# Kernel tuning notes

Hardware: AMD Instinct MI355X
Metric: run time of the kernel (lower is better)

## Reference

```python
import jax, jax.numpy as jnp
import numpy as np

EPS = 1e-6
CHUNK = 128  # chunk size for the causal linear-attention scan


def elu_plus_one(x):
    return jax.nn.elu(x) + 1.0


def causal_linear_attention(q, k, v):
    # out_t = (sq_t @ cumsum_{j<=t} sk_j v_j^T) / (sq_t . cumsum_{j<=t} sk_j), clamped
    B, S, D = q.shape
    sq = elu_plus_one(q)
    sk = elu_plus_one(k)
    N = S // CHUNK
    # [N, B, C, D] chunked layout for scan over chunks
    sq_c = sq.reshape(B, N, CHUNK, D).transpose(1, 0, 2, 3)
    sk_c = sk.reshape(B, N, CHUNK, D).transpose(1, 0, 2, 3)
    v_c = v.reshape(B, N, CHUNK, D).transpose(1, 0, 2, 3)
    mask = jnp.tril(jnp.ones((CHUNK, CHUNK), dtype=q.dtype))  # inclusive causal

    def step(carry, inp):
        S_kv, z = carry  # [B,D,D], [B,D] running sums from previous chunks
        sqi, ski, vi = inp
        A = jnp.einsum('bid,bjd->bij', sqi, ski) * mask  # intra-chunk causal scores
        num = jnp.einsum('bij,bje->bie', A, vi) + jnp.einsum('bid,bde->bie', sqi, S_kv)
        den = A.sum(-1) + jnp.einsum('bid,bd->bi', sqi, z)
        out = num / jnp.clip(den, EPS, None)[..., None]
        S_kv = S_kv + jnp.einsum('bcd,bce->bde', ski, vi)
        z = z + ski.sum(axis=1)
        return (S_kv, z), out

    init = (jnp.zeros((B, D, D), q.dtype), jnp.zeros((B, D), q.dtype))
    _, outs = jax.lax.scan(step, init, (sq_c, sk_c, v_c))
    return outs.transpose(1, 0, 2, 3).reshape(B, S, D)


def setup_inputs() -> dict:
    key = jax.random.key(0)
    ks = jax.random.split(key, 8)
    B, S, D = 2, 2048, 1024
    scale = 1.0 / np.sqrt(D)  # realistic init scale for the D x D projections
    return {
        'hidden_states': jax.random.normal(ks[0], (B, S, D), jnp.float32),
        'w_q': jax.random.normal(ks[1], (D, D), jnp.float32) * scale,
        'w_k': jax.random.normal(ks[2], (D, D), jnp.float32) * scale,
        'w_v': jax.random.normal(ks[3], (D, D), jnp.float32) * scale,
        'w_o': jax.random.normal(ks[4], (D, D), jnp.float32) * scale,
        'gate': jnp.zeros((1,), jnp.float32),
        'memory': jax.random.uniform(ks[5], (D, D), jnp.float32) * 0.01,
        'memory_norm': jax.random.uniform(ks[6], (D,), jnp.float32),
    }


def reference(hidden_states, w_q, w_k, w_v, w_o, gate, memory, memory_norm):
    # Projections (torch Linear: x @ W^T)
    q = hidden_states @ w_q.T
    k = hidden_states @ w_k.T
    v = hidden_states @ w_v.T

    # Retrieve from compressive memory (single bank)
    sigma_q = elu_plus_one(q)
    a_mem = sigma_q @ memory
    norm = jnp.clip(sigma_q @ memory_norm, EPS, None)[..., None]
    active = (memory_norm.sum() >= EPS).astype(q.dtype)
    memory_output = active * (a_mem / norm)

    local_output = causal_linear_attention(q, k, v)

    g = jax.nn.sigmoid(gate)  # [1], broadcasts
    output = g * memory_output + (1.0 - g) * local_output
    return output @ w_o.T
```

## Files before the change

### kernel.cpp

```cpp
#include <hip/hip_runtime.h>
#include <cstddef>

#define EPSF 1e-6f

constexpr int D   = 1024;
constexpr int Bv  = 2;
constexpr int S   = 2048;
constexpr int M   = Bv * S;
constexpr int CH  = 256;
constexpr int NCH = S / CH;

constexpr int TSZ  = 128 * 32;
constexpr int TA64 = 64 * 32;

typedef __attribute__((ext_vector_type(8))) short short8;
typedef __attribute__((ext_vector_type(4))) float floatx4;

__device__ __forceinline__ float elu1(float x) { return x > 0.f ? x + 1.f : __expf(x); }
__device__ __forceinline__ float sigmoidf_(float x) { return 1.f / (1.f + __expf(-x)); }
__device__ __forceinline__ unsigned short f2bf(float x) {
    unsigned u = __float_as_uint(x);
    return (unsigned short)((u + 0x7fffu + ((u >> 16) & 1u)) >> 16);
}
__device__ __forceinline__ float bf2f(unsigned short h) {
    return __uint_as_float(((unsigned)h) << 16);
}
__device__ __forceinline__ float wave_reduce(float x) {
#pragma unroll
    for (int off = 32; off > 0; off >>= 1) x += __shfl_down(x, off);
    return x;
}

__device__ __forceinline__ void gl_lds16(const unsigned short* g, unsigned short* l) {
    __builtin_amdgcn_global_load_lds(
        (const __attribute__((address_space(1))) void*)g,
        (__attribute__((address_space(3))) void*)l, 16, 0, 0);
}


__device__ __forceinline__ void stage128x32(const unsigned short* g, int stride,
                                            unsigned short* lds, int wave, int lane) {
    const int t   = (wave << 6) + lane;
    const int row = t >> 2;
    const int cb  = (((t & 3) ^ ((row >> 1) & 3)) << 3);
    unsigned short* l0 = lds + (wave << 9);
    gl_lds16(g + (size_t)row * stride + cb, l0);
    gl_lds16(g + (size_t)(row + 64) * stride + cb, l0 + 2048);
}

__device__ __forceinline__ void stage64x32(const unsigned short* g, int stride,
                                           unsigned short* lds, int wave, int lane) {
    const int t   = (wave << 6) + lane;
    const int row = t >> 2;
    const int cb  = (((t & 3) ^ ((row >> 1) & 3)) << 3);
    gl_lds16(g + (size_t)row * stride + cb, lds + (wave << 9));
}

__device__ __forceinline__ void mfma_step(const unsigned short* As, const unsigned short* Bs,
                                          int wm, int wn, int fr, int g, floatx4 acc[4][4]) {
    const int off = ((g ^ ((fr >> 1) & 3)) << 3);
    short8 af[4], bf[4];
#pragma unroll
    for (int i = 0; i < 4; ++i) af[i] = *(const short8*)&As[(wm + i * 16 + fr) * 32 + off];
#pragma unroll
    for (int j = 0; j < 4; ++j) bf[j] = *(const short8*)&Bs[(wn + j * 16 + fr) * 32 + off];
#pragma unroll
    for (int i = 0; i < 4; ++i)
#pragma unroll
        for (int j = 0; j < 4; ++j)
            acc[i][j] = __builtin_amdgcn_mfma_f32_16x16x32_bf16(af[i], bf[j], acc[i][j], 0, 0, 0);
}

__device__ __forceinline__ void mfma_step64d(const unsigned short* As, const unsigned short* Bs,
                                             int wm, int wn, int fr, int g,
                                             floatx4 acc[2][4], floatx4 accd[2], short8 bones) {
    const int off = ((g ^ ((fr >> 1) & 3)) << 3);
    short8 af[2], bf[4];
#pragma unroll
    for (int i = 0; i < 2; ++i) af[i] = *(const short8*)&As[(wm + i * 16 + fr) * 32 + off];
#pragma unroll
    for (int j = 0; j < 4; ++j) bf[j] = *(const short8*)&Bs[(wn + j * 16 + fr) * 32 + off];
#pragma unroll
    for (int i = 0; i < 2; ++i) {
#pragma unroll
        for (int j = 0; j < 4; ++j)
            acc[i][j] = __builtin_amdgcn_mfma_f32_16x16x32_bf16(af[i], bf[j], acc[i][j], 0, 0, 0);
        accd[i] = __builtin_amdgcn_mfma_f32_16x16x32_bf16(af[i], bones, accd[i], 0, 0, 0);
    }
}

__device__ __forceinline__ void mfma_step64(const unsigned short* As, const unsigned short* Bs,
                                            int wm, int wn, int fr, int g, floatx4 acc[2][4]) {
    const int off = ((g ^ ((fr >> 1) & 3)) << 3);
    short8 af[2], bf[4];
#pragma unroll
    for (int i = 0; i < 2; ++i) af[i] = *(const short8*)&As[(wm + i * 16 + fr) * 32 + off];
#pragma unroll
    for (int j = 0; j < 4; ++j) bf[j] = *(const short8*)&Bs[(wn + j * 16 + fr) * 32 + off];
#pragma unroll
    for (int i = 0; i < 2; ++i)
#pragma unroll
        for (int j = 0; j < 4; ++j)
            acc[i][j] = __builtin_amdgcn_mfma_f32_16x16x32_bf16(af[i], bf[j], acc[i][j], 0, 0, 0);
}

__device__ __forceinline__ void gemm_loop_db(const unsigned short* Ag, int strideA,
                                             const unsigned short* Bg, int strideB, int Kk,
                                             unsigned short* As, unsigned short* Bs,
                                             int wave, int lane, int wm, int wn, int fr, int g,
                                             floatx4 acc[4][4]) {
    __syncthreads();
    stage128x32(Ag, strideA, As, wave, lane);
    stage128x32(Bg, strideB, Bs, wave, lane);
    int buf = 0;
    for (int k0 = 32; k0 < Kk; k0 += 32) {
        __syncthreads();
        const int nb = buf ^ 1;
        stage128x32(Ag + k0, strideA, As + nb * TSZ, wave, lane);
        stage128x32(Bg + k0, strideB, Bs + nb * TSZ, wave, lane);
        mfma_step(As + buf * TSZ, Bs + buf * TSZ, wm, wn, fr, g, acc);
        buf = nb;
    }
    __syncthreads();
    mfma_step(As + buf * TSZ, Bs + buf * TSZ, wm, wn, fr, g, acc);
}

__device__ __forceinline__ void gemm_loop_db64d(const unsigned short* Ag, int strideA,
                                                const unsigned short* Bg, int strideB, int Kk,
                                                unsigned short* As, unsigned short* Bs,
                                                int wave, int lane, int wm, int wn, int fr, int g,
                                                floatx4 acc[2][4], floatx4 accd[2], short8 bones) {
    __syncthreads();
    stage64x32(Ag, strideA, As, wave, lane);
    stage128x32(Bg, strideB, Bs, wave, lane);
    int buf = 0;
    for (int k0 = 32; k0 < Kk; k0 += 32) {
        __syncthreads();
        const int nb = buf ^ 1;
        stage64x32(Ag + k0, strideA, As + nb * TA64, wave, lane);
        stage128x32(Bg + k0, strideB, Bs + nb * TSZ, wave, lane);
        mfma_step64d(As + buf * TA64, Bs + buf * TSZ, wm, wn, fr, g, acc, accd, bones);
        buf = nb;
    }
    __syncthreads();
    mfma_step64d(As + buf * TA64, Bs + buf * TSZ, wm, wn, fr, g, acc, accd, bones);
}

__device__ __forceinline__ void gemm_loop_db64(const unsigned short* Ag, int strideA,
                                               const unsigned short* Bg, int strideB, int Kk,
                                               unsigned short* As, unsigned short* Bs,
                                               int wave, int lane, int wm, int wn, int fr, int g,
                                               floatx4 acc[2][4]) {
    __syncthreads();
    stage64x32(Ag, strideA, As, wave, lane);
    stage128x32(Bg, strideB, Bs, wave, lane);
    int buf = 0;
    for (int k0 = 32; k0 < Kk; k0 += 32) {
        __syncthreads();
        const int nb = buf ^ 1;
        stage64x32(Ag + k0, strideA, As + nb * TA64, wave, lane);
        stage128x32(Bg + k0, strideB, Bs + nb * TSZ, wave, lane);
        mfma_step64(As + buf * TA64, Bs + buf * TSZ, wm, wn, fr, g, acc);
        buf = nb;
    }
    __syncthreads();
    mfma_step64(As + buf * TA64, Bs + buf * TSZ, wm, wn, fr, g, acc);
}

__global__ __launch_bounds__(256) void prep(const float* __restrict__ h,
                                            const float* __restrict__ w_q, const float* __restrict__ w_k,
                                            const float* __restrict__ w_v, const float* __restrict__ w_o,
                                            const float* __restrict__ memory,
                                            unsigned short* __restrict__ h_b,
                                            unsigned short* __restrict__ wq_b, unsigned short* __restrict__ wk_b,
                                            unsigned short* __restrict__ wv_b, unsigned short* __restrict__ wo_b,
                                            unsigned short* __restrict__ memT)
{
    __shared__ unsigned short T[64][72];
    const int id = blockIdx.x, tid = threadIdx.x;
    if (id < 4096) {
        const size_t i = ((size_t)id * 256 + tid) * 4;
        float4 v = *(const float4*)(h + i);
        ushort4 o; o.x = f2bf(v.x); o.y = f2bf(v.y); o.z = f2bf(v.z); o.w = f2bf(v.w);
        *(ushort4*)(h_b + i) = o;
    } else if (id < 8192) {
        const int t = id - 4096, which = t >> 10;
        const float* in = (which == 0) ? w_q : (which == 1) ? w_k : (which == 2) ? w_v : w_o;
        unsigned short* out = (which == 0) ? wq_b : (which == 1) ? wk_b : (which == 2) ? wv_b : wo_b;
        const size_t i = ((size_t)(t & 1023) * 256 + tid) * 4;
        float4 v = *(const float4*)(in + i);
        ushort4 o; o.x = f2bf(v.x); o.y = f2bf(v.y); o.z = f2bf(v.z); o.w = f2bf(v.w);
        *(ushort4*)(out + i) = o;
    } else {
        const int t = id - 8192;
        const int d0 = (t >> 4) * 64, e0 = (t & 15) * 64;
        const int r = tid >> 4, c4 = (tid & 15) * 4;
        for (int rr = r; rr < 64; rr += 16) {
            float4 v = *(const float4*)(memory + (size_t)(d0 + rr) * D + e0 + c4);
            T[rr][c4 + 0] = f2bf(v.x); T[rr][c4 + 1] = f2bf(v.y);
            T[rr][c4 + 2] = f2bf(v.z); T[rr][c4 + 3] = f2bf(v.w);
        }
        __syncthreads();
        for (int rr = r; rr < 64; rr += 16) {
            ushort4 o;
            o.x = T[c4 + 0][rr]; o.y = T[c4 + 1][rr];
            o.z = T[c4 + 2][rr]; o.w = T[c4 + 3][rr];
            *(ushort4*)(memT + (size_t)(e0 + rr) * D + d0 + c4) = o;
        }
    }
}

__global__ __launch_bounds__(256) void proj_fused(const unsigned short* __restrict__ h_b,
                                                  const unsigned short* __restrict__ wq,
                                                  const unsigned short* __restrict__ wk,
                                                  const unsigned short* __restrict__ wv,
                                                  unsigned short* __restrict__ sq,
                                                  unsigned short* __restrict__ sk,
                                                  unsigned short* __restrict__ v)
{
    __shared__ unsigned short As[2 * TSZ], Bs[2 * TSZ];
    const int id = blockIdx.x;
    const int x = id & 7, y = id >> 3;
    const int strip = x + 8 * (y % 12);
    const int n     = y / 12;
    const int sub = strip >> 5, m = strip & 31;
    const int m0 = m * 128, n0 = n * 128;
    const unsigned short* B = (sub == 0) ? wq : (sub == 1) ? wk : wv;
    unsigned short* C = (sub == 0) ? sq : (sub == 1) ? sk : v;

    const int tid = threadIdx.x, wave = tid >> 6, lane = tid & 63;
    const int wm = (wave >> 1) * 64, wn = (wave & 1) * 64;
    const int fr = lane & 15, g = lane >> 4;
    const int q4 = g * 4;

    floatx4 acc[4][4] = {};
    gemm_loop_db(h_b + (size_t)m0 * D, D, B + (size_t)n0 * D, D, D,
                 As, Bs, wave, lane, wm, wn, fr, g, acc);

#pragma unroll
    for (int i = 0; i < 4; ++i)
#pragma unroll
        for (int j = 0; j < 4; ++j) {
            const int col = n0 + wn + j * 16 + fr;
#pragma unroll
            for (int r = 0; r < 4; ++r) {
                const int row = m0 + wm + i * 16 + q4 + r;
                float val = acc[i][j][r];
                if (sub < 2) val = elu1(val);
                C[(size_t)row * D + col] = f2bf(val);
            }
        }
}

__global__ __launch_bounds__(256) void stage2(const unsigned short* __restrict__ sq,
                                              const unsigned short* __restrict__ sk,
                                              const unsigned short* __restrict__ memT,
                                              const unsigned short* __restrict__ v_b,
                                              const float* __restrict__ mnorm,
                                              const float* __restrict__ gate,
                                              unsigned short* __restrict__ combm,
                                              unsigned short* __restrict__ Sbuf2,
                                              unsigned short* __restrict__ vT,
                                              float* __restrict__ rowscale)
{
    __shared__ unsigned short As[2 * TSZ], Bs[2 * TSZ];
    const int id = blockIdx.x, tid = threadIdx.x;
    const int wave = tid >> 6, lane = tid & 63;
    const int wm = (wave >> 1) * 64, wn = (wave & 1) * 64;
    const int fr = lane & 15, g = lane >> 4;
    const int q4 = g * 4;

    if (id < 256) {
        const int x = id & 7, y = id >> 3;
        const int m0 = (x + 8 * (y & 3)) * 128;
        const int n0 = (y >> 2) * 128;
        floatx4 acc[4][4] = {};
        gemm_loop_db(sq + (size_t)m0 * D, D, memT + (size_t)n0 * D, D, D,
                     As, Bs, wave, lane, wm, wn, fr, g, acc);
#pragma unroll
        for (int i = 0; i < 4; ++i)
#pragma unroll
            for (int j = 0; j < 4; ++j) {
                const int col = n0 + wn + j * 16 + fr;
#pragma unroll
                for (int r = 0; r < 4; ++r)
                    combm[(size_t)(m0 + wm + i * 16 + q4 + r) * D + col] = f2bf(acc[i][j][r]);
            }
    } else if (id < 544) {
        const int t = id - 256;
        const int b = t / 144, rem = t % 144;
        const int p = rem >> 2, tt = rem & 3;
        const int it = tt >> 1, jt = tt & 1;
        int c = 0;
        while ((c + 1) * (c + 2) / 2 <= p) ++c;
        const int j = p - c * (c + 1) / 2;
        unsigned short* Srow0 = Sbuf2 + (size_t)(b * NCH + c) * CH * S;

        if (j == c && jt > it) {
            const int row = it * 128 + (tid >> 1);
            unsigned short* zp = Srow0 + (size_t)row * S + j * CH + jt * 128 + (tid & 1) * 64;
            uint4 z4 = make_uint4(0, 0, 0, 0);
#pragma unroll
            for (int i = 0; i < 8; ++i) *(uint4*)(zp + i * 8) = z4;
            return;
        }
        floatx4 acc[4][4] = {};
        gemm_loop_db(sq + ((size_t)b * S + (size_t)c * CH + it * 128) * D, D,
                     sk + ((size_t)b * S + (size_t)j * CH + jt * 128) * D, D, D,
                     As, Bs, wave, lane, wm, wn, fr, g, acc);
        const bool diag = (j == c && it == jt);
#pragma unroll
        for (int i = 0; i < 4; ++i)
#pragma unroll
            for (int jj = 0; jj < 4; ++jj) {
                const int col = jt * 128 + wn + jj * 16 + fr;
#pragma unroll
                for (int r = 0; r < 4; ++r) {
                    const int row = it * 128 + wm + i * 16 + q4 + r;
                    float val = acc[i][jj][r];
                    if (diag && col > row) val = 0.f;
                    Srow0[(size_t)row * S + j * CH + col] = f2bf(val);
                }
            }
    } else if (id < 1568) {
        unsigned short (*T)[72] = (unsigned short(*)[72])As;
        const int t = id - 544;
        const int b = t >> 9, rem = t & 511;
        const int s0 = (rem >> 4) * 64, d0 = (rem & 15) * 64;
        const int r = tid >> 4, c4 = (tid & 15) * 4;
        const unsigned short* ip = v_b + (size_t)b * S * D;
        for (int rr = r; rr < 64; rr += 16) {
            ushort4 vv = *(const ushort4*)(ip + (size_t)(s0 + rr) * D + d0 + c4);
            T[rr][c4 + 0] = vv.x; T[rr][c4 + 1] = vv.y; T[rr][c4 + 2] = vv.z; T[rr][c4 + 3] = vv.w;
        }
        __syncthreads();
        unsigned short* op = vT + (size_t)b * D * S;
        for (int rr = r; rr < 64; rr += 16) {
            ushort4 o;
            o.x = T[c4 + 0][rr]; o.y = T[c4 + 1][rr];
            o.z = T[c4 + 2][rr]; o.w = T[c4 + 3][rr];
            *(ushort4*)(op + (size_t)(d0 + rr) * S + s0 + c4) = o;
        }
    } else {
        const int row = (id - 1568) * 4 + wave;
        const unsigned short* sr = sq + (size_t)row * D;
        float dot = 0.f, msum = 0.f;
        for (int d = lane; d < D; d += 64) {
            float mn = mnorm[d];
            dot += bf2f(sr[d]) * mn;
            msum += mn;
        }
        dot = wave_reduce(dot);
        msum = wave_reduce(msum);
        if (lane == 0) {
            const float gg = sigmoidf_(gate[0]);
            const float active = (msum >= EPSF) ? 1.f : 0.f;
            rowscale[row] = gg * active / fmaxf(dot, EPSF);
        }
    }
}

__global__ __launch_bounds__(256) void pv64(const unsigned short* __restrict__ Sbuf2,
                                            const unsigned short* __restrict__ vT,
                                            const float* __restrict__ rowscale,
                                            const float* __restrict__ gate,
                                            unsigned short* __restrict__ combm)
{
    __shared__ unsigned short As2[2 * TA64], Bs2[2 * TSZ];
    const int id = blockIdx.x, tid = threadIdx.x;
    const int wave = tid >> 6, lane = tid & 63;
    const int wm = (wave >> 1) * 32, wn = (wave & 1) * 64;
    const int fr = lane & 15, g = lane >> 4;
    const int q4 = g * 4;

    const int x = id & 7, y = id >> 3;
    const int g_ = x + 8 * (y & 7);
    const int e  = y >> 3;
    const int b = g_ >> 5;
    const int rem = g_ & 31;
    const int c = (NCH - 1) - (rem >> 2);
    const int i0 = (rem & 3) * 64, e0 = e * 128;

    const short one_bf = (short)0x3F80;
    short8 bones = {one_bf, one_bf, one_bf, one_bf, one_bf, one_bf, one_bf, one_bf};

    floatx4 acc[2][4] = {};
    floatx4 accd[2] = {};
    gemm_loop_db64d(Sbuf2 + ((size_t)(b * NCH + c) * CH + i0) * S, S,
                    vT + (size_t)b * D * S + (size_t)e0 * S, S, (c + 1) * CH,
                    As2, Bs2, wave, lane, wm, wn, fr, g, acc, accd, bones);

    const float gg = sigmoidf_(gate[0]);
    const float wloc = 1.f - gg;
#pragma unroll
    for (int i = 0; i < 2; ++i)
#pragma unroll
        for (int j = 0; j < 4; ++j) {
            const int col = e0 + wn + j * 16 + fr;
#pragma unroll
            for (int r = 0; r < 4; ++r) {
                const int li = i0 + wm + i * 16 + q4 + r;
                const int rg = b * S + c * CH + li;
                const float inv = wloc / fmaxf(accd[i][r], EPSF);
                const size_t idx = (size_t)rg * D + col;
                combm[idx] = f2bf(bf2f(combm[idx]) * rowscale[rg] + acc[i][j][r] * inv);
            }
        }
}

__global__ __launch_bounds__(256) void outproj64(const unsigned short* __restrict__ A,
                                                 const unsigned short* __restrict__ wo,
                                                 float* __restrict__ out)
{
    __shared__ unsigned short As2[2 * TA64], Bs2[2 * TSZ];
    const int id = blockIdx.x, tid = threadIdx.x;
    const int wave = tid >> 6, lane = tid & 63;
    const int wm = (wave >> 1) * 32, wn = (wave & 1) * 64;
    const int fr = lane & 15, g = lane >> 4;
    const int q4 = g * 4;

    const int x = id & 7, y = id >> 3;
    const int m0 = (x + 8 * (y & 7)) * 64;
    const int n0 = (y >> 3) * 128;

    floatx4 acc[2][4] = {};
    gemm_loop_db64(A + (size_t)m0 * D, D, wo + (size_t)n0 * D, D, D,
                   As2, Bs2, wave, lane, wm, wn, fr, g, acc);

#pragma unroll
    for (int i = 0; i < 2; ++i)
#pragma unroll
        for (int j = 0; j < 4; ++j) {
            const int col = n0 + wn + j * 16 + fr;
#pragma unroll
            for (int r = 0; r < 4; ++r)
                out[(size_t)(m0 + wm + i * 16 + q4 + r) * D + col] = acc[i][j][r];
        }
}

extern "C" void kernel_launch(void* const* d_in, const int* in_sizes, int n_in,
                              void* d_out, int out_size, void* d_ws, size_t ws_size,
                              hipStream_t stream)
{
    const float* h      = (const float*)d_in[0];
    const float* w_q    = (const float*)d_in[1];
    const float* w_k    = (const float*)d_in[2];
    const float* w_v    = (const float*)d_in[3];
    const float* w_o    = (const float*)d_in[4];
    const float* gate   = (const float*)d_in[5];
    const float* memory = (const float*)d_in[6];
    const float* mnorm  = (const float*)d_in[7];
    float* out = (float*)d_out;

    unsigned short* h_b   = (unsigned short*)d_ws;
    unsigned short* wq_b  = h_b + (size_t)M * D;
    unsigned short* wk_b  = wq_b + (size_t)D * D;
    unsigned short* wv_b  = wk_b + (size_t)D * D;
    unsigned short* wo_b  = wv_b + (size_t)D * D;
    unsigned short* memT  = wo_b + (size_t)D * D;
    unsigned short* sq_b  = memT + (size_t)D * D;
    unsigned short* sk_b  = sq_b + (size_t)M * D;
    unsigned short* v_b   = sk_b + (size_t)M * D;
    unsigned short* vT    = v_b + (size_t)M * D;
    unsigned short* Sbuf2 = vT + (size_t)M * D;
    unsigned short* combm = Sbuf2 + (size_t)Bv * NCH * CH * S;
    float* rowscale = (float*)(combm + (size_t)M * D);

    dim3 blk(256);

    prep<<<8448, blk, 0, stream>>>(h, w_q, w_k, w_v, w_o, memory,
                                   h_b, wq_b, wk_b, wv_b, wo_b, memT);
    proj_fused<<<768, blk, 0, stream>>>(h_b, wq_b, wk_b, wv_b, sq_b, sk_b, v_b);
    stage2<<<2592, blk, 0, stream>>>(sq_b, sk_b, memT, v_b, mnorm, gate,
                                     combm, Sbuf2, vT, rowscale);
    pv64<<<512, blk, 0, stream>>>(Sbuf2, vT, rowscale, gate, combm);
    outproj64<<<512, blk, 0, stream>>>(combm, wo_b, out);
}
```

Measured before the change: 230.3 us.

## Replace QKV projection with 256x256-tile 8-wave GEMM using 128KB dynamic LDS

Adds a new projection kernel that computes 256x256 output tiles with 512 threads (8 waves, each 128x64). It uses 64-wide K steps, a double-buffered 128KB LDS pipeline staged via global_load_lds with XOR swizzle, interleaved prefetch, and setprio around the MFMA bursts. The larger tiles are meant to raise arithmetic intensity and cut global/LDS traffic compared with the 128x128 proj_fused, which is kept as a fallback if the large dynamic LDS request fails. Separately, the rowscale dot product is vectorized into 16-byte loads. Risks include low occupancy and only 192 blocks, which may underfill the CUs.

Result: no change. 227.2 us (-1.4%).

```diff
diff --git a/kernel.cpp b/kernel.cpp
--- a/kernel.cpp
+++ b/kernel.cpp
@@ -36,7 +36,6 @@
         (const __attribute__((address_space(1))) void*)g,
         (__attribute__((address_space(3))) void*)l, 16, 0, 0);
 }
-
 
 __device__ __forceinline__ void stage128x32(const unsigned short* g, int stride,
                                             unsigned short* lds, int wave, int lane) {
@@ -210,6 +209,122 @@
     }
 }
 
+__global__ __launch_bounds__(512, 2) void proj8(const unsigned short* __restrict__ h_b,
+                                                const unsigned short* __restrict__ wq,
+                                                const unsigned short* __restrict__ wk,
+                                                const unsigned short* __restrict__ wv,
+                                                unsigned short* __restrict__ sq,
+                                                unsigned short* __restrict__ sk,
+                                                unsigned short* __restrict__ v)
+{
+    extern __shared__ unsigned short sm[];
+    const int id = blockIdx.x;
+    const int x = id & 7, y = id >> 3;
+    const int strip = x + 8 * (y % 6);
+    const int nn = y / 6;
+    const int sub = strip >> 4, m = strip & 15;
+    const int m0 = m * 256, n0 = nn * 256;
+    const unsigned short* Ag = h_b + (size_t)m0 * D;
+    const unsigned short* Bg = ((sub == 0) ? wq : (sub == 1) ? wk : wv) + (size_t)n0 * D;
+    unsigned short* C = (sub == 0) ? sq : (sub == 1) ? sk : v;
+
+    const int tid = threadIdx.x;
+    const int w = tid >> 6, lane = tid & 63;
+    const int wr = w >> 2, wc = w & 3;
+    const int fr = lane & 15, gq = lane >> 4;
+    const int swz = fr & 7;
+
+    const int r0 = tid >> 3;
+    const int c0 = (tid & 7) ^ (r0 & 7);
+    const int r1 = (tid + 512) >> 3;
+    const int c1 = ((tid + 512) & 7) ^ (r1 & 7);
+    const size_t so0 = (size_t)r0 * D + (size_t)c0 * 8;
+    const size_t so1 = (size_t)r1 * D + (size_t)c1 * 8;
+    unsigned short* const dst0 = sm + tid * 8;
+    unsigned short* const dst1 = sm + (tid + 512) * 8;
+
+    floatx4 acc[8][4] = {};
+
+#define STG(kt, b, which) do {                                                      \
+        const unsigned short* Gs = ((which) < 2 ? Ag : Bg)                          \
+            + (size_t)(((which) & 1) * 128) * D + (size_t)(kt) * 64;                \
+        const int slot = (((b) << 2) + (which)) << 13;                              \
+        gl_lds16(Gs + so0, dst0 + slot);                                            \
+        gl_lds16(Gs + so1, dst1 + slot);                                            \
+    } while (0)
+
+    STG(0, 0, 0); STG(0, 0, 1); STG(0, 0, 2); STG(0, 0, 3);
+    STG(1, 1, 2); STG(1, 1, 3);
+    asm volatile("s_waitcnt vmcnt(4)" ::: "memory");
+    __builtin_amdgcn_s_barrier();
+
+    const int NT = D / 64;
+    for (int u = 0; u < NT; ++u) {
+        const int bu = u & 1;
+        const unsigned short* Ah = sm + (((bu << 2) + wr) << 13);
+        const unsigned short* Bh = sm + (((bu << 2) + 2 + (wc >> 1)) << 13);
+        const int brow = (wc & 1) * 64;
+        short8 bfr[4][2];
+#pragma unroll
+        for (int s = 0; s < 4; ++s) {
+            short8 afr[2][2];
+#pragma unroll
+            for (int i2 = 0; i2 < 2; ++i2)
+#pragma unroll
+                for (int ks = 0; ks < 2; ++ks)
+                    afr[i2][ks] = *(const short8*)&Ah[((s * 2 + i2) * 16 + fr) * 64
+                                                      + ((((ks << 2) + gq) ^ swz) << 3)];
+            if (s == 0) {
+#pragma unroll
+                for (int j = 0; j < 4; ++j)
+#pragma unroll
+                    for (int ks = 0; ks < 2; ++ks)
+                        bfr[j][ks] = *(const short8*)&Bh[(brow + j * 16 + fr) * 64
+                                                         + ((((ks << 2) + gq) ^ swz) << 3)];
+            }
+            if (s == 0)      { if (u + 1 < NT) STG(u + 1, bu ^ 1, 0); }
+            else if (s == 1) { if (u + 1 < NT) STG(u + 1, bu ^ 1, 1); }
+            else if (s == 2) { if (u + 2 < NT) STG(u + 2, bu, 2); }
+            else {
+                if (u + 2 < NT) {
+                    STG(u + 2, bu, 3);
+                    asm volatile("s_waitcnt vmcnt(4)" ::: "memory");
+                } else if (u + 1 < NT) {
+                    asm volatile("s_waitcnt vmcnt(0)" ::: "memory");
+                }
+            }
+            __builtin_amdgcn_s_barrier();
+            __builtin_amdgcn_s_setprio(1);
+#pragma unroll
+            for (int i2 = 0; i2 < 2; ++i2)
+#pragma unroll
+                for (int j = 0; j < 4; ++j)
+#pragma unroll
+                    for (int ks = 0; ks < 2; ++ks)
+                        acc[s * 2 + i2][j] = __builtin_amdgcn_mfma_f32_16x16x32_bf16(
+                            afr[i2][ks], bfr[j][ks], acc[s * 2 + i2][j], 0, 0, 0);
+            __builtin_amdgcn_s_setprio(0);
+            __builtin_amdgcn_s_barrier();
+        }
+    }
+#undef STG
+
+    const int q4 = gq * 4;
+#pragma unroll
+    for (int i = 0; i < 8; ++i)
+#pragma unroll
+        for (int j = 0; j < 4; ++j) {
+            const int col = n0 + wc * 64 + j * 16 + fr;
+#pragma unroll
+            for (int r = 0; r < 4; ++r) {
+                const int row = m0 + wr * 128 + i * 16 + q4 + r;
+                float val = acc[i][j][r];
+                if (sub < 2) val = elu1(val);
+                C[(size_t)row * D + col] = f2bf(val);
+            }
+        }
+}
+
 __global__ __launch_bounds__(256) void proj_fused(const unsigned short* __restrict__ h_b,
                                                   const unsigned short* __restrict__ wq,
                                                   const unsigned short* __restrict__ wk,
@@ -345,10 +460,17 @@
         const int row = (id - 1568) * 4 + wave;
         const unsigned short* sr = sq + (size_t)row * D;
         float dot = 0.f, msum = 0.f;
-        for (int d = lane; d < D; d += 64) {
-            float mn = mnorm[d];
-            dot += bf2f(sr[d]) * mn;
-            msum += mn;
+#pragma unroll
+        for (int p = 0; p < 2; ++p) {
+            const int d0 = p * 512 + lane * 8;
+            short8 sv = *(const short8*)(sr + d0);
+            float4 m0 = *(const float4*)(mnorm + d0);
+            float4 m1 = *(const float4*)(mnorm + d0 + 4);
+            dot += bf2f((unsigned short)sv[0]) * m0.x + bf2f((unsigned short)sv[1]) * m0.y
+                 + bf2f((unsigned short)sv[2]) * m0.z + bf2f((unsigned short)sv[3]) * m0.w
+                 + bf2f((unsigned short)sv[4]) * m1.x + bf2f((unsigned short)sv[5]) * m1.y
+                 + bf2f((unsigned short)sv[6]) * m1.z + bf2f((unsigned short)sv[7]) * m1.w;
+            msum += m0.x + m0.y + m0.z + m0.w + m1.x + m1.y + m1.z + m1.w;
         }
         dot = wave_reduce(dot);
         msum = wave_reduce(msum);
@@ -470,7 +592,17 @@
 
     prep<<<8448, blk, 0, stream>>>(h, w_q, w_k, w_v, w_o, memory,
                                    h_b, wq_b, wk_b, wv_b, wo_b, memT);
-    proj_fused<<<768, blk, 0, stream>>>(h_b, wq_b, wk_b, wv_b, sq_b, sk_b, v_b);
+
+    static const bool proj8_ok = [] {
+        return hipFuncSetAttribute(reinterpret_cast<const void*>(proj8),
+                                   hipFuncAttributeMaxDynamicSharedMemorySize,
+                                   131072) == hipSuccess;
+    }();
+    if (proj8_ok)
+        proj8<<<192, dim3(512), 131072, stream>>>(h_b, wq_b, wk_b, wv_b, sq_b, sk_b, v_b);
+    else
+        proj_fused<<<768, blk, 0, stream>>>(h_b, wq_b, wk_b, wv_b, sq_b, sk_b, v_b);
+
     stage2<<<2592, blk, 0, stream>>>(sq_b, sk_b, memT, v_b, mnorm, gate,
                                      combm, Sbuf2, vT, rowscale);
     pv64<<<512, blk, 0, stream>>>(Sbuf2, vT, rowscale, gate, combm);
```
